# Kernel tuning notes

Measured on AMD Instinct MI355X. Metric: run time of the kernel, lower is better.

Reference implementation:

```python
import jax, jax.numpy as jnp
import numpy as np

NHEAD = 16
NEG1 = -9e15   # first masked_fill value (-9000000000000000.0)
NEG2 = -9e16   # second masked_fill value


def setup_inputs() -> dict:
    key = jax.random.key(0)
    ks = jax.random.split(key, 8)
    slen, bsz, emb = 512, 16, 1024
    x = jax.random.normal(ks[0], (slen, bsz, emb), dtype=jnp.float32)
    mask = jax.random.randint(ks[1], (bsz, slen, slen), 0, 2, dtype=jnp.int32)
    weight_mask = jax.random.randint(ks[2], (bsz, slen, slen), 0, 2, dtype=jnp.int32)
    s = 1.0 / np.sqrt(emb)
    Wq = jax.random.normal(ks[3], (emb, emb), dtype=jnp.float32) * s
    Wk = jax.random.normal(ks[4], (emb, emb), dtype=jnp.float32) * s
    Wv = jax.random.normal(ks[5], (emb, emb), dtype=jnp.float32) * s
    Ws = jax.random.normal(ks[6], (emb, emb), dtype=jnp.float32) * s
    Wb = jax.random.normal(ks[7], (1, 3 * emb), dtype=jnp.float32) * s
    return {"x": x, "mask": mask, "weight_mask": weight_mask,
            "Wq": Wq, "Wk": Wk, "Wv": Wv, "Ws": Ws, "Wb": Wb}


def reference(x, mask, weight_mask, Wq, Wk, Wv, Ws, Wb):
    slen, bsz, emb = x.shape
    hd = emb // NHEAD
    scaling = float(hd) ** -0.5

    def split_heads(t):  # (slen, bsz, emb) -> (bsz, nhead, slen, hd)
        return t.reshape(slen, bsz, NHEAD, hd).transpose(1, 2, 0, 3)

    q = split_heads(x @ Wq.T)
    k = split_heads(x @ Wk.T)
    v = split_heads(x @ Wv.T)

    attn = jnp.einsum('bhqd,bhkd->bhqk', q, k) * scaling

    m = mask.astype(attn.dtype)[:, None, :, :]          # (bsz,1,slen,slen)
    attn = jnp.where(m == 0, NEG1, attn)
    attn = jax.nn.softmax(attn, axis=-1) * m

    wm = weight_mask.astype(attn.dtype)[:, None, :, :]
    attn = jnp.where(wm == 0, NEG2, attn)
    attn = jax.nn.softmax(attn, axis=-1) * wm
    # degree normalization: row-normalize
    attn = attn * (1.0 / (attn.sum(-1) + 1e-10))[..., None]

    # dropout inactive (eval mode)
    out = jnp.einsum('bhqk,bhkd->bhqd', attn, v)         # (bsz,nhead,slen,hd)
    out = out.transpose(2, 0, 1, 3).reshape(slen, bsz, emb)

    r = x @ Ws.T
    gate = jax.nn.sigmoid(jnp.concatenate([out, r, out - r], axis=-1) @ Wb.T)
    return gate * r + (1.0 - gate) * out
```

## Files before the change

kernel.cpp:

```cpp
#include <hip/hip_runtime.h>
#include <hip/hip_bf16.h>
#include <stdint.h>

typedef __attribute__((ext_vector_type(8))) short short8;
typedef __attribute__((ext_vector_type(4))) float f32x4;
typedef __attribute__((ext_vector_type(4))) unsigned short ushort4v;

#define MFMA_BF16(a,b,c) __builtin_amdgcn_mfma_f32_16x16x32_bf16((a),(b),(c),0,0,0)

static __device__ __forceinline__ unsigned short f2bf(float f){
  union { float fv; unsigned int u; } c; c.fv = f;
  unsigned int u = c.u;
  return (unsigned short)((u + 0x7fffu + ((u >> 16) & 1u)) >> 16);
}

static __device__ __forceinline__ unsigned int cvtpk(float a, float b){
  unsigned int r;
  asm("v_cvt_pk_bf16_f32 %0, %1, %2" : "=v"(r) : "v"(a), "v"(b));
  return r;
}

static __device__ __forceinline__ void gload_lds16(const void* g, void* l){
  __builtin_amdgcn_global_load_lds(
      (const __attribute__((address_space(1))) void*)g,
      (__attribute__((address_space(3))) void*)l, 16, 0, 0);
}

static __device__ __forceinline__ float wred_sum(float v){
  #pragma unroll
  for (int m = 32; m; m >>= 1) v += __shfl_xor(v, m, 64);
  return v;
}

static __device__ __forceinline__ void unpack8(uint4 u, float* f){
  f[0] = __uint_as_float(u.x << 16); f[1] = __uint_as_float(u.x & 0xFFFF0000u);
  f[2] = __uint_as_float(u.y << 16); f[3] = __uint_as_float(u.y & 0xFFFF0000u);
  f[4] = __uint_as_float(u.z << 16); f[5] = __uint_as_float(u.z & 0xFFFF0000u);
  f[6] = __uint_as_float(u.w << 16); f[7] = __uint_as_float(u.w & 0xFFFF0000u);
}

__global__ __launch_bounds__(256) void cvt_x_kernel(const float* __restrict__ x,
                                                    unsigned short* __restrict__ o){
  int i = blockIdx.x * 256 + threadIdx.x;
  float4 f = ((const float4*)x)[i];
  ushort4v r;
  r[0] = f2bf(f.x); r[1] = f2bf(f.y); r[2] = f2bf(f.z); r[3] = f2bf(f.w);
  ((ushort4v*)o)[i] = r;
}

__global__ __launch_bounds__(256) void cvt_w_kernel(const float* __restrict__ Wq,
                                                    const float* __restrict__ Wk,
                                                    const float* __restrict__ Wv,
                                                    const float* __restrict__ Ws,
                                                    unsigned short* __restrict__ B){
  int i = blockIdx.x * 256 + threadIdx.x;
  int which = i >> 18;
  const float* src = (which == 0) ? Wq : (which == 1) ? Wk : (which == 2) ? Wv : Ws;
  float4 f = ((const float4*)src)[i & 262143];
  ushort4v r;
  r[0] = f2bf(f.x); r[1] = f2bf(f.y); r[2] = f2bf(f.z); r[3] = f2bf(f.w);
  ((ushort4v*)B)[i] = r;
}

__global__ void wb_prep_kernel(const float* __restrict__ Wb,
                               float* __restrict__ wba, float* __restrict__ wbb){
  int e = blockIdx.x * 256 + threadIdx.x;
  if (e < 1024){
    wba[e] = Wb[e]        + Wb[2048 + e];
    wbb[e] = Wb[1024 + e] - Wb[2048 + e];
  }
}

__global__ __launch_bounds__(256) void mask_prep_kernel(
    const int* __restrict__ m, const int* __restrict__ wm,
    unsigned long long* __restrict__ mb, unsigned long long* __restrict__ wb)
{
  const size_t i = (size_t)blockIdx.x * 256 + threadIdx.x;
  const int a = m[i];
  const int c = wm[i];
  unsigned long long ba = __ballot(a != 0);
  unsigned long long bc = __ballot(c != 0);
  if ((threadIdx.x & 63) == 0){
    mb[i >> 6] = ba;
    wb[i >> 6] = bc;
  }
}

__global__ __launch_bounds__(256, 3) void gemm_proj_kernel(
    const unsigned short* __restrict__ X, const unsigned short* __restrict__ B,
    unsigned short* __restrict__ qb, unsigned short* __restrict__ kb,
    unsigned short* __restrict__ vT, float* __restrict__ rb)
{
  __shared__ __align__(16) unsigned short smem[128 * 136];
  unsigned short* As = smem;
  unsigned short* Bs = smem + 4096;
  const int tid = threadIdx.x;
  const int w = tid >> 6, l = tid & 63;
  const int lr = l & 15, lq = l >> 4;
  const int wr = w >> 1, wc = w & 1;
  const int bid = ((blockIdx.x & 7) << 8) | (blockIdx.x >> 3);
  const int m0 = (bid >> 5) * 128;
  const int n0 = (bid & 31) * 128;
  f32x4 acc[4][4] = {};

  for (int k0 = 0; k0 < 1024; k0 += 32){
    #pragma unroll
    for (int i = 0; i < 2; i++){
      int c = i * 256 + tid;
      gload_lds16(X + (size_t)(m0 + (c >> 2)) * 1024 + k0 + (c & 3) * 8,
                  As + (i * 256 + w * 64) * 8);
      gload_lds16(B + (size_t)(n0 + (c >> 2)) * 1024 + k0 + (c & 3) * 8,
                  Bs + (i * 256 + w * 64) * 8);
    }
    __syncthreads();
    short8 av[4], bv[4];
    #pragma unroll
    for (int mf = 0; mf < 4; mf++)
      av[mf] = *(const short8*)(As + (wr * 64 + mf * 16 + lr) * 32 + lq * 8);
    #pragma unroll
    for (int nf = 0; nf < 4; nf++)
      bv[nf] = *(const short8*)(Bs + (wc * 64 + nf * 16 + lr) * 32 + lq * 8);
    #pragma unroll
    for (int mf = 0; mf < 4; mf++)
      #pragma unroll
      for (int nf = 0; nf < 4; nf++)
        acc[mf][nf] = MFMA_BF16(av[mf], bv[nf], acc[mf][nf]);
    __syncthreads();
  }

  const int which = (n0 >> 10);
  if (which == 3){
    #pragma unroll
    for (int mf = 0; mf < 4; mf++)
      #pragma unroll
      for (int nf = 0; nf < 4; nf++){
        const int o = (n0 & 1023) + wc * 64 + nf * 16 + lr;
        #pragma unroll
        for (int rg = 0; rg < 4; rg++){
          const int rowi = m0 + wr * 64 + mf * 16 + lq * 4 + rg;
          rb[(size_t)rowi * 1024 + o] = acc[mf][nf][rg];
        }
      }
  } else if (which == 2){
    #pragma unroll
    for (int mf = 0; mf < 4; mf++)
      #pragma unroll
      for (int nf = 0; nf < 4; nf++){
        const int r0 = wr * 64 + mf * 16 + lq * 4;
        const int c  = wc * 64 + nf * 16 + lr;
        uint2 pk;
        pk.x = cvtpk(acc[mf][nf][0], acc[mf][nf][1]);
        pk.y = cvtpk(acc[mf][nf][2], acc[mf][nf][3]);
        *(uint2*)(smem + c * 132 + r0) = pk;
      }
    __syncthreads();
    const int s0 = m0 >> 4;
    #pragma unroll
    for (int p = 0; p < 8; p++){
      const int cid = p * 256 + tid;
      const int c = cid >> 4, bb = cid & 15;
      short8 st;
      #pragma unroll
      for (int j = 0; j < 8; j++) st[j] = (short)smem[c * 132 + j * 16 + bb];
      const int o = (n0 & 1023) + c;
      const int bh = bb * 16 + (o >> 6), d = o & 63;
      *(short8*)(vT + ((size_t)bh * 64 + d) * 512 + s0) = st;
    }
  } else {
    #pragma unroll
    for (int mf = 0; mf < 4; mf++)
      #pragma unroll
      for (int nf = 0; nf < 4; nf++)
        #pragma unroll
        for (int rg = 0; rg < 4; rg++)
          smem[(wr * 64 + mf * 16 + lq * 4 + rg) * 136 + wc * 64 + nf * 16 + lr]
              = f2bf(acc[mf][nf][rg]);
    __syncthreads();
    unsigned short* dst = (which == 0) ? qb : kb;
    #pragma unroll
    for (int p = 0; p < 8; p++){
      const int cid = p * 256 + tid;
      const int lrow = cid >> 4, cg = cid & 15;
      short8 vv = *(const short8*)(smem + lrow * 136 + cg * 8);
      const int rowi = m0 + lrow;
      const int s = rowi >> 4, bb = rowi & 15;
      const int o = (n0 & 1023) + cg * 8;
      const int bh = bb * 16 + (o >> 6), d = o & 63;
      *(short8*)(dst + ((size_t)bh * 512 + s) * 64 + d) = vv;
    }
  }
}

__global__ __launch_bounds__(256, 4) void attn_kernel(
    const unsigned short* __restrict__ qg, const unsigned short* __restrict__ kg,
    const unsigned short* __restrict__ vt,
    const unsigned char* __restrict__ mbits, const unsigned char* __restrict__ wbits,
    float* __restrict__ outp)
{
  __shared__ __align__(16) unsigned short sE[32 * 520];
  __shared__ float sfin[32];
  const int bid = ((blockIdx.x & 7) << 9) | (blockIdx.x >> 3);
  const int qt = bid & 15, h = (bid >> 4) & 15, b = bid >> 8;
  const int tid = threadIdx.x, w = tid >> 6, l = tid & 63;
  const int lr = l & 15, lq = l >> 4;
  const int bh = b * 16 + h;
  const unsigned short* qp = qg + ((size_t)bh * 512 + qt * 32) * 64;
  const unsigned short* kp = kg + (size_t)bh * 512 * 64;
  const unsigned short* vp = vt + (size_t)bh * 64 * 512;

  const unsigned char* mrb = mbits + ((size_t)(b * 512 + qt * 32)) * 64;
  const unsigned char* wrb = wbits + ((size_t)(b * 512 + qt * 32)) * 64;
  unsigned int mby[2][4], wby[2][4];
  #pragma unroll
  for (int g = 0; g < 2; g++)
    #pragma unroll
    for (int rr = 0; rr < 4; rr++){
      mby[g][rr] = mrb[(g * 16 + w * 4 + rr) * 64 + l];
      wby[g][rr] = wrb[(g * 16 + w * 4 + rr) * 64 + l];
    }

  short8 qa[2][2];
  #pragma unroll
  for (int t = 0; t < 2; t++){
    qa[t][0] = *(const short8*)(qp + (t * 16 + lr) * 64 + lq * 8);
    qa[t][1] = *(const short8*)(qp + (t * 16 + lr) * 64 + 32 + lq * 8);
  }
  const float CEXP = 0.18033688011112042f;
  #pragma unroll
  for (int kf = 0; kf < 8; kf++){
    const unsigned short* kr = kp + (size_t)(w * 128 + kf * 16 + lr) * 64;
    short8 k0 = *(const short8*)(kr + lq * 8);
    short8 k1 = *(const short8*)(kr + 32 + lq * 8);
    f32x4 a0 = {}, a1 = {};
    a0 = MFMA_BF16(qa[0][0], k0, a0);
    a1 = MFMA_BF16(qa[1][0], k0, a1);
    a0 = MFMA_BF16(qa[0][1], k1, a0);
    a1 = MFMA_BF16(qa[1][1], k1, a1);
    const int col = w * 128 + kf * 16 + lr;
    #pragma unroll
    for (int t = 0; t < 2; t++){
      f32x4 a = t ? a1 : a0;
      float e0 = __builtin_amdgcn_exp2f(a[0] * CEXP);
      float e1 = __builtin_amdgcn_exp2f(a[1] * CEXP);
      float e2 = __builtin_amdgcn_exp2f(a[2] * CEXP);
      float e3 = __builtin_amdgcn_exp2f(a[3] * CEXP);
      unsigned int p01 = cvtpk(e0, e1), p23 = cvtpk(e2, e3);
      const int row = t * 16 + lq * 4;
      sE[(row    ) * 520 + col] = (unsigned short)(p01 & 0xFFFFu);
      sE[(row + 1) * 520 + col] = (unsigned short)(p01 >> 16);
      sE[(row + 2) * 520 + col] = (unsigned short)(p23 & 0xFFFFu);
      sE[(row + 3) * 520 + col] = (unsigned short)(p23 >> 16);
    }
  }
  __syncthreads();

  #pragma unroll
  for (int g = 0; g < 2; g++){
    const int row0 = g * 16 + w * 4;
    uint4 ev[4];
    #pragma unroll
    for (int rr = 0; rr < 4; rr++)
      ev[rr] = *(const uint4*)(sE + (row0 + rr) * 520 + l * 8);

    float em[4][8]; float z1[4];
    #pragma unroll
    for (int rr = 0; rr < 4; rr++){
      float e1[8];
      unpack8(ev[rr], e1);
      const unsigned int mb = mby[g][rr];
      float z = 0.f;
      #pragma unroll
      for (int j = 0; j < 8; j++){
        em[rr][j] = ((mb >> j) & 1u) ? e1[j] : 0.f;
        z += em[rr][j];
      }
      z1[rr] = z;
    }
    #pragma unroll
    for (int m = 32; m; m >>= 1){
      #pragma unroll
      for (int rr = 0; rr < 4; rr++) z1[rr] += __shfl_xor(z1[rr], m, 64);
    }
    float e2[4][8]; float z2[4];
    #pragma unroll
    for (int rr = 0; rr < 4; rr++){
      const float i1L = 1.4426950408889634f / z1[rr];
      const unsigned int wv = wby[g][rr];
      float z = 0.f;
      #pragma unroll
      for (int j = 0; j < 8; j++){
        float t = __builtin_amdgcn_exp2f(em[rr][j] * i1L);
        e2[rr][j] = ((wv >> j) & 1u) ? t : 0.f;
        z += e2[rr][j];
      }
      z2[rr] = z;
    }
    #pragma unroll
    for (int m = 32; m; m >>= 1){
      #pragma unroll
      for (int rr = 0; rr < 4; rr++) z2[rr] += __shfl_xor(z2[rr], m, 64);
    }
    #pragma unroll
    for (int rr = 0; rr < 4; rr++){
      uint4 o;
      o.x = cvtpk(e2[rr][0], e2[rr][1]); o.y = cvtpk(e2[rr][2], e2[rr][3]);
      o.z = cvtpk(e2[rr][4], e2[rr][5]); o.w = cvtpk(e2[rr][6], e2[rr][7]);
      *(uint4*)(sE + (row0 + rr) * 520 + l * 8) = o;
      if (l == 0) sfin[row0 + rr] = 1.f / (z2[rr] + 1e-10f);
    }
  }
  __syncthreads();

  {
    f32x4 po0 = {}, po1 = {};
    #pragma unroll
    for (int ks = 0; ks < 16; ks++){
      short8 vf = *(const short8*)(vp + (size_t)(w * 16 + lr) * 512 + ks * 32 + lq * 8);
      short8 af0 = *(const short8*)(sE + (     lr) * 520 + ks * 32 + lq * 8);
      short8 af1 = *(const short8*)(sE + (16 + lr) * 520 + ks * 32 + lq * 8);
      po0 = MFMA_BF16(af0, vf, po0);
      po1 = MFMA_BF16(af1, vf, po1);
    }
    #pragma unroll
    for (int rg = 0; rg < 4; rg++){
      const int r0 = lq * 4 + rg;
      outp[((size_t)(qt * 32 + r0) * 16 + b) * 1024 + h * 64 + w * 16 + lr]
          = po0[rg] * sfin[r0];
      outp[((size_t)(qt * 32 + 16 + r0) * 16 + b) * 1024 + h * 64 + w * 16 + lr]
          = po1[rg] * sfin[16 + r0];
    }
  }
}

__global__ __launch_bounds__(256) void gate_kernel(
    const float* __restrict__ outp, const float* __restrict__ rb,
    const float* __restrict__ wba, const float* __restrict__ wbb,
    float* __restrict__ y)
{
  const int t = blockIdx.x * 4 + (threadIdx.x >> 6);
  const int l = threadIdx.x & 63;
  const float* o = outp + (size_t)t * 1024;
  const float* r = rb + (size_t)t * 1024;
  float ov[16], rv[16];
  float acc = 0.f;
  #pragma unroll
  for (int j = 0; j < 16; j++){
    const int e = j * 64 + l;
    ov[j] = o[e]; rv[j] = r[e];
    acc += ov[j] * wba[e] + rv[j] * wbb[e];
  }
  const float dot = wred_sum(acc);
  const float g = 1.f / (1.f + __builtin_amdgcn_exp2f(-dot * 1.4426950408889634f));
  float* yo = y + (size_t)t * 1024;
  #pragma unroll
  for (int j = 0; j < 16; j++){
    const int e = j * 64 + l;
    yo[e] = g * rv[j] + (1.f - g) * ov[j];
  }
}

extern "C" void kernel_launch(void* const* d_in, const int* in_sizes, int n_in,
                              void* d_out, int out_size, void* d_ws, size_t ws_size,
                              hipStream_t stream)
{
  (void)in_sizes; (void)n_in; (void)out_size; (void)ws_size;
  const float* x   = (const float*)d_in[0];
  const int* mask  = (const int*)d_in[1];
  const int* wmask = (const int*)d_in[2];
  const float* Wq  = (const float*)d_in[3];
  const float* Wk  = (const float*)d_in[4];
  const float* Wv  = (const float*)d_in[5];
  const float* Ws  = (const float*)d_in[6];
  const float* Wb  = (const float*)d_in[7];

  char* ws = (char*)d_ws;
  unsigned short* xbf = (unsigned short*)ws; ws += 16777216;
  unsigned short* bm  = (unsigned short*)ws; ws += 8388608;
  unsigned short* qb  = (unsigned short*)ws; ws += 16777216;
  unsigned short* kb  = (unsigned short*)ws; ws += 16777216;
  unsigned short* vT  = (unsigned short*)ws; ws += 16777216;
  float* rb  = (float*)ws; ws += 33554432;
  float* op  = (float*)ws; ws += 33554432;
  float* wba = (float*)ws; ws += 4096;
  float* wbb = (float*)ws; ws += 4096;
  unsigned long long* mb64 = (unsigned long long*)xbf;
  unsigned long long* wb64 = (unsigned long long*)bm;

  cvt_x_kernel<<<8192, 256, 0, stream>>>(x, xbf);
  cvt_w_kernel<<<4096, 256, 0, stream>>>(Wq, Wk, Wv, Ws, bm);
  wb_prep_kernel<<<4, 256, 0, stream>>>(Wb, wba, wbb);
  gemm_proj_kernel<<<2048, 256, 0, stream>>>(xbf, bm, qb, kb, vT, rb);
  mask_prep_kernel<<<16384, 256, 0, stream>>>(mask, wmask, mb64, wb64);
  attn_kernel<<<4096, 256, 0, stream>>>(qb, kb, vT,
      (const unsigned char*)mb64, (const unsigned char*)wb64, op);
  gate_kernel<<<2048, 256, 0, stream>>>(op, rb, wba, wbb, (float*)d_out);
}
```

Baseline: 208.8 us.

## Enlarge projection GEMM tile to 256x128 with 512 threads; store attention output as bf16

```diff
diff --git a/kernel.cpp b/kernel.cpp
--- a/kernel.cpp
+++ b/kernel.cpp
@@ -86,32 +86,30 @@
   }
 }
 
-__global__ __launch_bounds__(256, 3) void gemm_proj_kernel(
+__global__ __launch_bounds__(512, 4) void gemm_proj_kernel(
     const unsigned short* __restrict__ X, const unsigned short* __restrict__ B,
     unsigned short* __restrict__ qb, unsigned short* __restrict__ kb,
     unsigned short* __restrict__ vT, float* __restrict__ rb)
 {
-  __shared__ __align__(16) unsigned short smem[128 * 136];
+  __shared__ __align__(16) unsigned short smem[17408];
   unsigned short* As = smem;
-  unsigned short* Bs = smem + 4096;
+  unsigned short* Bs = smem + 8192;
   const int tid = threadIdx.x;
   const int w = tid >> 6, l = tid & 63;
   const int lr = l & 15, lq = l >> 4;
   const int wr = w >> 1, wc = w & 1;
-  const int bid = ((blockIdx.x & 7) << 8) | (blockIdx.x >> 3);
-  const int m0 = (bid >> 5) * 128;
-  const int n0 = (bid & 31) * 128;
+  const int bid = ((blockIdx.x & 7) << 7) | (blockIdx.x >> 3);
+  const int nt = bid >> 5, mt = bid & 31;
+  const int m0 = mt * 256, n0 = nt * 128;
   f32x4 acc[4][4] = {};
 
   for (int k0 = 0; k0 < 1024; k0 += 32){
-    #pragma unroll
-    for (int i = 0; i < 2; i++){
-      int c = i * 256 + tid;
-      gload_lds16(X + (size_t)(m0 + (c >> 2)) * 1024 + k0 + (c & 3) * 8,
-                  As + (i * 256 + w * 64) * 8);
-      gload_lds16(B + (size_t)(n0 + (c >> 2)) * 1024 + k0 + (c & 3) * 8,
-                  Bs + (i * 256 + w * 64) * 8);
-    }
+    gload_lds16(X + (size_t)(m0 + (tid >> 2)) * 1024 + k0 + (tid & 3) * 8,
+                As + (w * 64) * 8);
+    gload_lds16(X + (size_t)(m0 + 128 + (tid >> 2)) * 1024 + k0 + (tid & 3) * 8,
+                As + (512 + w * 64) * 8);
+    gload_lds16(B + (size_t)(n0 + (tid >> 2)) * 1024 + k0 + (tid & 3) * 8,
+                Bs + (w * 64) * 8);
     __syncthreads();
     short8 av[4], bv[4];
     #pragma unroll
@@ -128,13 +126,14 @@
     __syncthreads();
   }
 
-  const int which = (n0 >> 10);
+  const int which = nt >> 3;
+  const int o0 = n0 & 1023;
   if (which == 3){
     #pragma unroll
     for (int mf = 0; mf < 4; mf++)
       #pragma unroll
       for (int nf = 0; nf < 4; nf++){
-        const int o = (n0 & 1023) + wc * 64 + nf * 16 + lr;
+        const int o = o0 + wc * 64 + nf * 16 + lr;
         #pragma unroll
         for (int rg = 0; rg < 4; rg++){
           const int rowi = m0 + wr * 64 + mf * 16 + lq * 4 + rg;
@@ -143,50 +142,62 @@
       }
   } else if (which == 2){
     #pragma unroll
-    for (int mf = 0; mf < 4; mf++)
-      #pragma unroll
-      for (int nf = 0; nf < 4; nf++){
-        const int r0 = wr * 64 + mf * 16 + lq * 4;
-        const int c  = wc * 64 + nf * 16 + lr;
-        uint2 pk;
-        pk.x = cvtpk(acc[mf][nf][0], acc[mf][nf][1]);
-        pk.y = cvtpk(acc[mf][nf][2], acc[mf][nf][3]);
-        *(uint2*)(smem + c * 132 + r0) = pk;
-      }
-    __syncthreads();
-    const int s0 = m0 >> 4;
-    #pragma unroll
-    for (int p = 0; p < 8; p++){
-      const int cid = p * 256 + tid;
-      const int c = cid >> 4, bb = cid & 15;
-      short8 st;
-      #pragma unroll
-      for (int j = 0; j < 8; j++) st[j] = (short)smem[c * 132 + j * 16 + bb];
-      const int o = (n0 & 1023) + c;
-      const int bh = bb * 16 + (o >> 6), d = o & 63;
-      *(short8*)(vT + ((size_t)bh * 64 + d) * 512 + s0) = st;
+    for (int ch = 0; ch < 2; ch++){
+      __syncthreads();
+      if (wc == ch){
+        #pragma unroll
+        for (int mf = 0; mf < 4; mf++)
+          #pragma unroll
+          for (int nf = 0; nf < 4; nf++){
+            const int cl = nf * 16 + lr;
+            const int r0 = wr * 64 + mf * 16 + lq * 4;
+            uint2 pk;
+            pk.x = cvtpk(acc[mf][nf][0], acc[mf][nf][1]);
+            pk.y = cvtpk(acc[mf][nf][2], acc[mf][nf][3]);
+            *(uint2*)(smem + cl * 264 + r0) = pk;
+          }
+      }
+      __syncthreads();
+      #pragma unroll
+      for (int p = 0; p < 4; p++){
+        const int cid = p * 512 + tid;
+        const int cl = cid >> 5, bb = (cid >> 1) & 15, sh = cid & 1;
+        short8 st;
+        #pragma unroll
+        for (int jj = 0; jj < 8; jj++)
+          st[jj] = (short)smem[cl * 264 + (sh * 8 + jj) * 16 + bb];
+        const int o = o0 + ch * 64 + cl;
+        const int bh = bb * 16 + (o >> 6), d = o & 63;
+        *(short8*)(vT + ((size_t)bh * 64 + d) * 512 + (m0 >> 4) + sh * 8) = st;
+      }
     }
   } else {
-    #pragma unroll
-    for (int mf = 0; mf < 4; mf++)
-      #pragma unroll
-      for (int nf = 0; nf < 4; nf++)
+    unsigned short* dst = which ? kb : qb;
+    #pragma unroll
+    for (int h2 = 0; h2 < 2; h2++){
+      __syncthreads();
+      if ((wr >> 1) == h2){
         #pragma unroll
-        for (int rg = 0; rg < 4; rg++)
-          smem[(wr * 64 + mf * 16 + lq * 4 + rg) * 136 + wc * 64 + nf * 16 + lr]
-              = f2bf(acc[mf][nf][rg]);
-    __syncthreads();
-    unsigned short* dst = (which == 0) ? qb : kb;
-    #pragma unroll
-    for (int p = 0; p < 8; p++){
-      const int cid = p * 256 + tid;
-      const int lrow = cid >> 4, cg = cid & 15;
-      short8 vv = *(const short8*)(smem + lrow * 136 + cg * 8);
-      const int rowi = m0 + lrow;
-      const int s = rowi >> 4, bb = rowi & 15;
-      const int o = (n0 & 1023) + cg * 8;
-      const int bh = bb * 16 + (o >> 6), d = o & 63;
-      *(short8*)(dst + ((size_t)bh * 512 + s) * 64 + d) = vv;
+        for (int mf = 0; mf < 4; mf++)
+          #pragma unroll
+          for (int nf = 0; nf < 4; nf++)
+            #pragma unroll
+            for (int rg = 0; rg < 4; rg++)
+              smem[((wr & 1) * 64 + mf * 16 + lq * 4 + rg) * 136 + wc * 64 + nf * 16 + lr]
+                  = f2bf(acc[mf][nf][rg]);
+      }
+      __syncthreads();
+      #pragma unroll
+      for (int p = 0; p < 4; p++){
+        const int cid = p * 512 + tid;
+        const int lrow = cid >> 4, cg = cid & 15;
+        short8 vv = *(const short8*)(smem + lrow * 136 + cg * 8);
+        const int rowi = m0 + h2 * 128 + lrow;
+        const int s = rowi >> 4, bb2 = rowi & 15;
+        const int o = o0 + cg * 8;
+        const int bh = bb2 * 16 + (o >> 6), d = o & 63;
+        *(short8*)(dst + ((size_t)bh * 512 + s) * 64 + d) = vv;
+      }
     }
   }
 }
@@ -195,7 +206,7 @@
     const unsigned short* __restrict__ qg, const unsigned short* __restrict__ kg,
     const unsigned short* __restrict__ vt,
     const unsigned char* __restrict__ mbits, const unsigned char* __restrict__ wbits,
-    float* __restrict__ outp)
+    unsigned short* __restrict__ outp)
 {
   __shared__ __align__(16) unsigned short sE[32 * 520];
   __shared__ float sfin[32];
@@ -325,28 +336,29 @@
     for (int rg = 0; rg < 4; rg++){
       const int r0 = lq * 4 + rg;
       outp[((size_t)(qt * 32 + r0) * 16 + b) * 1024 + h * 64 + w * 16 + lr]
-          = po0[rg] * sfin[r0];
+          = f2bf(po0[rg] * sfin[r0]);
       outp[((size_t)(qt * 32 + 16 + r0) * 16 + b) * 1024 + h * 64 + w * 16 + lr]
-          = po1[rg] * sfin[16 + r0];
+          = f2bf(po1[rg] * sfin[16 + r0]);
     }
   }
 }
 
 __global__ __launch_bounds__(256) void gate_kernel(
-    const float* __restrict__ outp, const float* __restrict__ rb,
+    const unsigned short* __restrict__ outp, const float* __restrict__ rb,
     const float* __restrict__ wba, const float* __restrict__ wbb,
     float* __restrict__ y)
 {
   const int t = blockIdx.x * 4 + (threadIdx.x >> 6);
   const int l = threadIdx.x & 63;
-  const float* o = outp + (size_t)t * 1024;
+  const unsigned short* o = outp + (size_t)t * 1024;
   const float* r = rb + (size_t)t * 1024;
   float ov[16], rv[16];
   float acc = 0.f;
   #pragma unroll
   for (int j = 0; j < 16; j++){
     const int e = j * 64 + l;
-    ov[j] = o[e]; rv[j] = r[e];
+    ov[j] = __uint_as_float((unsigned int)o[e] << 16);
+    rv[j] = r[e];
     acc += ov[j] * wba[e] + rv[j] * wbb[e];
   }
   const float dot = wred_sum(acc);
@@ -380,7 +392,7 @@
   unsigned short* kb  = (unsigned short*)ws; ws += 16777216;
   unsigned short* vT  = (unsigned short*)ws; ws += 16777216;
   float* rb  = (float*)ws; ws += 33554432;
-  float* op  = (float*)ws; ws += 33554432;
+  unsigned short* op = (unsigned short*)ws; ws += 33554432;
   float* wba = (float*)ws; ws += 4096;
   float* wbb = (float*)ws; ws += 4096;
   unsigned long long* mb64 = (unsigned long long*)xbf;
@@ -389,7 +401,7 @@
   cvt_x_kernel<<<8192, 256, 0, stream>>>(x, xbf);
   cvt_w_kernel<<<4096, 256, 0, stream>>>(Wq, Wk, Wv, Ws, bm);
   wb_prep_kernel<<<4, 256, 0, stream>>>(Wb, wba, wbb);
-  gemm_proj_kernel<<<2048, 256, 0, stream>>>(xbf, bm, qb, kb, vT, rb);
+  gemm_proj_kernel<<<1024, 512, 0, stream>>>(xbf, bm, qb, kb, vT, rb);
   mask_prep_kernel<<<16384, 256, 0, stream>>>(mask, wmask, mb64, wb64);
   attn_kernel<<<4096, 256, 0, stream>>>(qb, kb, vT,
       (const unsigned char*)mb64, (const unsigned char*)wb64, op);
```

Measured after the change: 198.2 us. -5.1%, faster.

## Store attention output and residual projection in bf16, swizzle GEMM LDS tiles

Applied to the files above, without the earlier changes.

```diff
diff --git a/kernel.cpp b/kernel.cpp
--- a/kernel.cpp
+++ b/kernel.cpp
@@ -86,10 +86,10 @@
   }
 }
 
-__global__ __launch_bounds__(256, 3) void gemm_proj_kernel(
+__global__ __launch_bounds__(256, 4) void gemm_proj_kernel(
     const unsigned short* __restrict__ X, const unsigned short* __restrict__ B,
     unsigned short* __restrict__ qb, unsigned short* __restrict__ kb,
-    unsigned short* __restrict__ vT, float* __restrict__ rb)
+    unsigned short* __restrict__ vT, unsigned short* __restrict__ rbb)
 {
   __shared__ __align__(16) unsigned short smem[128 * 136];
   unsigned short* As = smem;
@@ -101,25 +101,28 @@
   const int bid = ((blockIdx.x & 7) << 8) | (blockIdx.x >> 3);
   const int m0 = (bid >> 5) * 128;
   const int n0 = (bid & 31) * 128;
+  const int gsw = (lr >> 1) & 3;
   f32x4 acc[4][4] = {};
 
   for (int k0 = 0; k0 < 1024; k0 += 32){
     #pragma unroll
     for (int i = 0; i < 2; i++){
-      int c = i * 256 + tid;
-      gload_lds16(X + (size_t)(m0 + (c >> 2)) * 1024 + k0 + (c & 3) * 8,
+      const int c = i * 256 + tid;
+      const int row = c >> 2;
+      const int cgs = (c & 3) ^ ((c >> 3) & 3);
+      gload_lds16(X + (size_t)(m0 + row) * 1024 + k0 + cgs * 8,
                   As + (i * 256 + w * 64) * 8);
-      gload_lds16(B + (size_t)(n0 + (c >> 2)) * 1024 + k0 + (c & 3) * 8,
+      gload_lds16(B + (size_t)(n0 + row) * 1024 + k0 + cgs * 8,
                   Bs + (i * 256 + w * 64) * 8);
     }
     __syncthreads();
     short8 av[4], bv[4];
     #pragma unroll
     for (int mf = 0; mf < 4; mf++)
-      av[mf] = *(const short8*)(As + (wr * 64 + mf * 16 + lr) * 32 + lq * 8);
+      av[mf] = *(const short8*)(As + (wr * 64 + mf * 16 + lr) * 32 + (lq ^ gsw) * 8);
     #pragma unroll
     for (int nf = 0; nf < 4; nf++)
-      bv[nf] = *(const short8*)(Bs + (wc * 64 + nf * 16 + lr) * 32 + lq * 8);
+      bv[nf] = *(const short8*)(Bs + (wc * 64 + nf * 16 + lr) * 32 + (lq ^ gsw) * 8);
     #pragma unroll
     for (int mf = 0; mf < 4; mf++)
       #pragma unroll
@@ -129,19 +132,8 @@
   }
 
   const int which = (n0 >> 10);
-  if (which == 3){
-    #pragma unroll
-    for (int mf = 0; mf < 4; mf++)
-      #pragma unroll
-      for (int nf = 0; nf < 4; nf++){
-        const int o = (n0 & 1023) + wc * 64 + nf * 16 + lr;
-        #pragma unroll
-        for (int rg = 0; rg < 4; rg++){
-          const int rowi = m0 + wr * 64 + mf * 16 + lq * 4 + rg;
-          rb[(size_t)rowi * 1024 + o] = acc[mf][nf][rg];
-        }
-      }
-  } else if (which == 2){
+  const int o0 = n0 & 1023;
+  if (which == 2){
     #pragma unroll
     for (int mf = 0; mf < 4; mf++)
       #pragma unroll
@@ -162,7 +154,7 @@
       short8 st;
       #pragma unroll
       for (int j = 0; j < 8; j++) st[j] = (short)smem[c * 132 + j * 16 + bb];
-      const int o = (n0 & 1023) + c;
+      const int o = o0 + c;
       const int bh = bb * 16 + (o >> 6), d = o & 63;
       *(short8*)(vT + ((size_t)bh * 64 + d) * 512 + s0) = st;
     }
@@ -176,17 +168,27 @@
           smem[(wr * 64 + mf * 16 + lq * 4 + rg) * 136 + wc * 64 + nf * 16 + lr]
               = f2bf(acc[mf][nf][rg]);
     __syncthreads();
-    unsigned short* dst = (which == 0) ? qb : kb;
-    #pragma unroll
-    for (int p = 0; p < 8; p++){
-      const int cid = p * 256 + tid;
-      const int lrow = cid >> 4, cg = cid & 15;
-      short8 vv = *(const short8*)(smem + lrow * 136 + cg * 8);
-      const int rowi = m0 + lrow;
-      const int s = rowi >> 4, bb = rowi & 15;
-      const int o = (n0 & 1023) + cg * 8;
-      const int bh = bb * 16 + (o >> 6), d = o & 63;
-      *(short8*)(dst + ((size_t)bh * 512 + s) * 64 + d) = vv;
+    if (which == 3){
+      #pragma unroll
+      for (int p = 0; p < 8; p++){
+        const int cid = p * 256 + tid;
+        const int lrow = cid >> 4, cg = cid & 15;
+        short8 vv = *(const short8*)(smem + lrow * 136 + cg * 8);
+        *(short8*)(rbb + (size_t)(m0 + lrow) * 1024 + o0 + cg * 8) = vv;
+      }
+    } else {
+      unsigned short* dst = (which == 0) ? qb : kb;
+      #pragma unroll
+      for (int p = 0; p < 8; p++){
+        const int cid = p * 256 + tid;
+        const int lrow = cid >> 4, cg = cid & 15;
+        short8 vv = *(const short8*)(smem + lrow * 136 + cg * 8);
+        const int rowi = m0 + lrow;
+        const int s = rowi >> 4, bb = rowi & 15;
+        const int o = o0 + cg * 8;
+        const int bh = bb * 16 + (o >> 6), d = o & 63;
+        *(short8*)(dst + ((size_t)bh * 512 + s) * 64 + d) = vv;
+      }
     }
   }
 }
@@ -195,7 +197,7 @@
     const unsigned short* __restrict__ qg, const unsigned short* __restrict__ kg,
     const unsigned short* __restrict__ vt,
     const unsigned char* __restrict__ mbits, const unsigned char* __restrict__ wbits,
-    float* __restrict__ outp)
+    unsigned short* __restrict__ outp)
 {
   __shared__ __align__(16) unsigned short sE[32 * 520];
   __shared__ float sfin[32];
@@ -325,28 +327,29 @@
     for (int rg = 0; rg < 4; rg++){
       const int r0 = lq * 4 + rg;
       outp[((size_t)(qt * 32 + r0) * 16 + b) * 1024 + h * 64 + w * 16 + lr]
-          = po0[rg] * sfin[r0];
+          = f2bf(po0[rg] * sfin[r0]);
       outp[((size_t)(qt * 32 + 16 + r0) * 16 + b) * 1024 + h * 64 + w * 16 + lr]
-          = po1[rg] * sfin[16 + r0];
+          = f2bf(po1[rg] * sfin[16 + r0]);
     }
   }
 }
 
 __global__ __launch_bounds__(256) void gate_kernel(
-    const float* __restrict__ outp, const float* __restrict__ rb,
+    const unsigned short* __restrict__ outp, const unsigned short* __restrict__ rbb,
     const float* __restrict__ wba, const float* __restrict__ wbb,
     float* __restrict__ y)
 {
   const int t = blockIdx.x * 4 + (threadIdx.x >> 6);
   const int l = threadIdx.x & 63;
-  const float* o = outp + (size_t)t * 1024;
-  const float* r = rb + (size_t)t * 1024;
+  const unsigned short* o = outp + (size_t)t * 1024;
+  const unsigned short* r = rbb + (size_t)t * 1024;
   float ov[16], rv[16];
   float acc = 0.f;
   #pragma unroll
   for (int j = 0; j < 16; j++){
     const int e = j * 64 + l;
-    ov[j] = o[e]; rv[j] = r[e];
+    ov[j] = __uint_as_float((unsigned int)o[e] << 16);
+    rv[j] = __uint_as_float((unsigned int)r[e] << 16);
     acc += ov[j] * wba[e] + rv[j] * wbb[e];
   }
   const float dot = wred_sum(acc);
@@ -379,8 +382,8 @@
   unsigned short* qb  = (unsigned short*)ws; ws += 16777216;
   unsigned short* kb  = (unsigned short*)ws; ws += 16777216;
   unsigned short* vT  = (unsigned short*)ws; ws += 16777216;
-  float* rb  = (float*)ws; ws += 33554432;
-  float* op  = (float*)ws; ws += 33554432;
+  unsigned short* rbb = (unsigned short*)ws; ws += 16777216;
+  unsigned short* op  = (unsigned short*)ws; ws += 16777216;
   float* wba = (float*)ws; ws += 4096;
   float* wbb = (float*)ws; ws += 4096;
   unsigned long long* mb64 = (unsigned long long*)xbf;
@@ -389,9 +392,9 @@
   cvt_x_kernel<<<8192, 256, 0, stream>>>(x, xbf);
   cvt_w_kernel<<<4096, 256, 0, stream>>>(Wq, Wk, Wv, Ws, bm);
   wb_prep_kernel<<<4, 256, 0, stream>>>(Wb, wba, wbb);
-  gemm_proj_kernel<<<2048, 256, 0, stream>>>(xbf, bm, qb, kb, vT, rb);
+  gemm_proj_kernel<<<2048, 256, 0, stream>>>(xbf, bm, qb, kb, vT, rbb);
   mask_prep_kernel<<<16384, 256, 0, stream>>>(mask, wmask, mb64, wb64);
   attn_kernel<<<4096, 256, 0, stream>>>(qb, kb, vT,
       (const unsigned char*)mb64, (const unsigned char*)wb64, op);
-  gate_kernel<<<2048, 256, 0, stream>>>(op, rb, wba, wbb, (float*)d_out);
-}
+  gate_kernel<<<2048, 256, 0, stream>>>(op, rbb, wba, wbb, (float*)d_out);
+}
```

Result: faster. 201.8 us (-3.4%).
